# Kernel optimization log

Measured on AMD Instinct MI355X. Metric: run time of the kernel, lower is better.

Reference implementation:

```python
import jax, jax.numpy as jnp
import numpy as np

QUEST_DIM = 768
C, X, Y = 2048, 19, 19
B = 64

def setup_inputs() -> dict:
    key = jax.random.key(0)
    k1, k2, k3, k4 = jax.random.split(key, 4)
    text_fts = jax.random.normal(k1, (B, QUEST_DIM), dtype=jnp.float32)
    img_fts = jax.random.normal(k2, (B, C, X, Y), dtype=jnp.float32)
    # Linear params (PyTorch nn.Linear: y = x @ W.T + b)
    bound = 1.0 / np.sqrt(QUEST_DIM)
    W = jax.random.uniform(k3, (C, QUEST_DIM), minval=-bound, maxval=bound, dtype=jnp.float32)
    b = jax.random.uniform(k4, (C,), minval=-bound, maxval=bound, dtype=jnp.float32)
    return {"text_fts": text_fts, "img_fts": img_fts, "W": W, "b": b}

def reference(text_fts, img_fts, W, b):
    batch = text_fts.shape[0]
    q = text_fts @ W.T + b                      # [B, C]
    img_flat = img_fts.reshape(batch, C, X * Y) # [B, C, S]
    sims = jnp.einsum('bc,bcs->bs', q, img_flat)  # dot over channel dim
    weights = jax.nn.softmax(sims, axis=1)        # softmax over spatial locations
    final_ans = jnp.einsum('bcs,bs->bc', img_flat, weights)  # weighted pooling
    return final_ans
```

## Files before the change

### kernel.cpp

```cpp
#include <hip/hip_runtime.h>
#include <math.h>

#define Bsz  64
#define Cch  2048
#define Kdim 768
#define Ssp  361

__global__ __launch_bounds__(256) void k_qgemm(
    const float* __restrict__ text, const float* __restrict__ W,
    const float* __restrict__ bias, float* __restrict__ qT)
{
    const int lane = threadIdx.x & 63;
    const int wv   = threadIdx.x >> 6;
    const int c0   = blockIdx.x * 8 + wv * 2;
    const int b0   = blockIdx.y * 16;

    const float4* wA = (const float4*)(W + (size_t)c0 * Kdim);
    const float4* wB = (const float4*)(W + (size_t)(c0 + 1) * Kdim);
    const float4 a0 = wA[lane*3+0], a1 = wA[lane*3+1], a2 = wA[lane*3+2];
    const float4 b0v = wB[lane*3+0], b1v = wB[lane*3+1], b2v = wB[lane*3+2];
    const float biasA = bias[c0], biasB = bias[c0 + 1];

    for (int b = b0; b < b0 + 16; b++) {
        const float4* t = (const float4*)(text + (size_t)b * Kdim);
        const float4 t0 = t[lane*3+0], t1 = t[lane*3+1], t2 = t[lane*3+2];
        float r0 = a0.x*t0.x + a0.y*t0.y + a0.z*t0.z + a0.w*t0.w
                 + a1.x*t1.x + a1.y*t1.y + a1.z*t1.z + a1.w*t1.w
                 + a2.x*t2.x + a2.y*t2.y + a2.z*t2.z + a2.w*t2.w;
        float r1 = b0v.x*t0.x + b0v.y*t0.y + b0v.z*t0.z + b0v.w*t0.w
                 + b1v.x*t1.x + b1v.y*t1.y + b1v.z*t1.z + b1v.w*t1.w
                 + b2v.x*t2.x + b2v.y*t2.y + b2v.z*t2.z + b2v.w*t2.w;
        #pragma unroll
        for (int off = 32; off; off >>= 1) {
            r0 += __shfl_xor(r0, off);
            r1 += __shfl_xor(r1, off);
        }
        if (lane == 0) {
            qT[(size_t)c0 * Bsz + b]       = r0 + biasA;
            qT[(size_t)(c0 + 1) * Bsz + b] = r1 + biasB;
        }
    }
}

__global__ __launch_bounds__(384) void k_sims(
    const float* __restrict__ img, const float* __restrict__ qT,
    float* __restrict__ sims_part)
{
    const int b  = blockIdx.x;
    const int cg = blockIdx.y;
    const int tid = threadIdx.x;

    __shared__ float qL[128];
    if (tid < 128) qL[tid] = qT[(size_t)(cg * 128 + tid) * Bsz + b];
    __syncthreads();

    if (tid < Ssp) {
        const float* base = img + ((size_t)b * Cch + (size_t)cg * 128) * Ssp + tid;
        float acc = 0.f;
        #pragma unroll 8
        for (int c = 0; c < 128; c++)
            acc += qL[c] * base[(size_t)c * Ssp];
        sims_part[((size_t)b * 16 + cg) * Ssp + tid] = acc;
    }
}

__global__ __launch_bounds__(384) void k_wts(
    const float* __restrict__ sims_part, float* __restrict__ wts)
{
    const int b   = blockIdx.x;
    const int tid = threadIdx.x;
    const int lane = tid & 63;
    const int wv   = tid >> 6;

    __shared__ float red[6];

    float s0 = -1e30f;
    if (tid < Ssp) {
        float a = 0.f;
        #pragma unroll
        for (int g = 0; g < 16; g++)
            a += sims_part[((size_t)b * 16 + g) * Ssp + tid];
        s0 = a;
    }

    float m = s0;
    #pragma unroll
    for (int off = 32; off; off >>= 1) m = fmaxf(m, __shfl_xor(m, off));
    if (lane == 0) red[wv] = m;
    __syncthreads();
    m = red[0];
    #pragma unroll
    for (int w = 1; w < 6; w++) m = fmaxf(m, red[w]);
    __syncthreads();

    const float e0 = (tid < Ssp) ? __expf(s0 - m) : 0.f;
    float l = e0;
    #pragma unroll
    for (int off = 32; off; off >>= 1) l += __shfl_xor(l, off);
    if (lane == 0) red[wv] = l;
    __syncthreads();
    l = red[0] + red[1] + red[2] + red[3] + red[4] + red[5];

    if (tid < Ssp)
        wts[(size_t)b * Ssp + tid] = e0 / l;
}

__global__ __launch_bounds__(256) void k_pool(
    const float* __restrict__ img, const float* __restrict__ wts,
    float* __restrict__ out)
{
    const int b   = blockIdx.x;
    const int cg  = blockIdx.y;
    const int tid = threadIdx.x;
    const int lane = tid & 63;
    const int wv   = tid >> 6;

    __shared__ float w[Ssp];
    __shared__ float outL[64];

    if (tid < Ssp)       w[tid]       = wts[(size_t)b * Ssp + tid];
    if (tid + 256 < Ssp) w[tid + 256] = wts[(size_t)b * Ssp + tid + 256];
    __syncthreads();

    for (int c = wv; c < 64; c += 4) {
        const float* base = img + ((size_t)b * Cch + (size_t)cg * 64 + c) * Ssp;
        float p = 0.f;
        #pragma unroll
        for (int j = 0; j < 5; j++)
            p += base[lane + 64 * j] * w[lane + 64 * j];
        if (lane + 320 < Ssp)
            p += base[lane + 320] * w[lane + 320];
        #pragma unroll
        for (int off = 32; off; off >>= 1) p += __shfl_xor(p, off);
        if (lane == 0) outL[c] = p;
    }
    __syncthreads();
    if (tid < 64)
        out[(size_t)b * Cch + (size_t)cg * 64 + tid] = outL[tid];
}

extern "C" void kernel_launch(void* const* d_in, const int* in_sizes, int n_in,
                              void* d_out, int out_size, void* d_ws, size_t ws_size,
                              hipStream_t stream) {
    const float* text = (const float*)d_in[0];
    const float* img  = (const float*)d_in[1];
    const float* W    = (const float*)d_in[2];
    const float* bias = (const float*)d_in[3];
    float* out = (float*)d_out;

    float* qT        = (float*)d_ws;
    float* sims_part = qT + (size_t)Cch * Bsz;
    float* wts       = sims_part + (size_t)Bsz * 16 * Ssp;

    k_qgemm<<<dim3(256, 4), 256, 0, stream>>>(text, W, bias, qT);
    k_sims <<<dim3(Bsz, 16), 384, 0, stream>>>(img, qT, sims_part);
    k_wts  <<<dim3(Bsz),     384, 0, stream>>>(sims_part, wts);
    k_pool <<<dim3(Bsz, 32), 256, 0, stream>>>(img, wts, out);
}
```

Baseline: 318.7 us.

## Fuse softmax into sims kernel via last-block atomic counter; widen pool and qgemm grids

The softmax kernel is folded into the sims kernel: each block bumps a per-batch atomic counter, and the last of the 16 channel-group blocks reduces the partial sims and writes the softmax weights. This removes one kernel launch and its dependency gap, at the cost of a memset on the counters and threadfences. The qgemm grid is doubled so each block handles 8 batches instead of 16. The pool kernel moves to 512-thread blocks that each handle 128 channels, with two channels per wave iteration so each weight read from shared memory is reused.

```diff
diff --git a/kernel.cpp b/kernel.cpp
--- a/kernel.cpp
+++ b/kernel.cpp
@@ -13,7 +13,7 @@
     const int lane = threadIdx.x & 63;
     const int wv   = threadIdx.x >> 6;
     const int c0   = blockIdx.x * 8 + wv * 2;
-    const int b0   = blockIdx.y * 16;
+    const int b0   = blockIdx.y * 8;
 
     const float4* wA = (const float4*)(W + (size_t)c0 * Kdim);
     const float4* wB = (const float4*)(W + (size_t)(c0 + 1) * Kdim);
@@ -21,7 +21,7 @@
     const float4 b0v = wB[lane*3+0], b1v = wB[lane*3+1], b2v = wB[lane*3+2];
     const float biasA = bias[c0], biasB = bias[c0 + 1];
 
-    for (int b = b0; b < b0 + 16; b++) {
+    for (int b = b0; b < b0 + 8; b++) {
         const float4* t = (const float4*)(text + (size_t)b * Kdim);
         const float4 t0 = t[lane*3+0], t1 = t[lane*3+1], t2 = t[lane*3+2];
         float r0 = a0.x*t0.x + a0.y*t0.y + a0.z*t0.z + a0.w*t0.w
@@ -44,7 +44,8 @@
 
 __global__ __launch_bounds__(384) void k_sims(
     const float* __restrict__ img, const float* __restrict__ qT,
-    float* __restrict__ sims_part)
+    float* __restrict__ sims_part, float* __restrict__ wts,
+    int* __restrict__ cnt)
 {
     const int b  = blockIdx.x;
     const int cg = blockIdx.y;
@@ -62,16 +63,19 @@
             acc += qL[c] * base[(size_t)c * Ssp];
         sims_part[((size_t)b * 16 + cg) * Ssp + tid] = acc;
     }
-}
 
-__global__ __launch_bounds__(384) void k_wts(
-    const float* __restrict__ sims_part, float* __restrict__ wts)
-{
-    const int b   = blockIdx.x;
-    const int tid = threadIdx.x;
+    __syncthreads();
+    __shared__ int isLast;
+    if (tid == 0) {
+        __threadfence();
+        isLast = (atomicAdd(&cnt[b], 1) == 15);
+    }
+    __syncthreads();
+    if (!isLast) return;
+    __threadfence();
+
     const int lane = tid & 63;
     const int wv   = tid >> 6;
-
     __shared__ float red[6];
 
     float s0 = -1e30f;
@@ -105,7 +109,7 @@
         wts[(size_t)b * Ssp + tid] = e0 / l;
 }
 
-__global__ __launch_bounds__(256) void k_pool(
+__global__ __launch_bounds__(512) void k_pool(
     const float* __restrict__ img, const float* __restrict__ wts,
     float* __restrict__ out)
 {
@@ -116,27 +120,41 @@
     const int wv   = tid >> 6;
 
     __shared__ float w[Ssp];
-    __shared__ float outL[64];
+    __shared__ float outL[128];
 
-    if (tid < Ssp)       w[tid]       = wts[(size_t)b * Ssp + tid];
-    if (tid + 256 < Ssp) w[tid + 256] = wts[(size_t)b * Ssp + tid + 256];
+    if (tid < Ssp) w[tid] = wts[(size_t)b * Ssp + tid];
     __syncthreads();
 
-    for (int c = wv; c < 64; c += 4) {
-        const float* base = img + ((size_t)b * Cch + (size_t)cg * 64 + c) * Ssp;
-        float p = 0.f;
+    const int cbase = cg * 128 + wv * 16;
+    #pragma unroll 2
+    for (int cc = 0; cc < 16; cc += 2) {
+        const float* base0 = img + ((size_t)b * Cch + cbase + cc) * Ssp;
+        const float* base1 = base0 + Ssp;
+        float p0 = 0.f, p1 = 0.f;
         #pragma unroll
-        for (int j = 0; j < 5; j++)
-            p += base[lane + 64 * j] * w[lane + 64 * j];
-        if (lane + 320 < Ssp)
-            p += base[lane + 320] * w[lane + 320];
+        for (int j = 0; j < 5; j++) {
+            const float wj = w[lane + 64 * j];
+            p0 += base0[lane + 64 * j] * wj;
+            p1 += base1[lane + 64 * j] * wj;
+        }
+        if (lane + 320 < Ssp) {
+            const float wt = w[lane + 320];
+            p0 += base0[lane + 320] * wt;
+            p1 += base1[lane + 320] * wt;
+        }
         #pragma unroll
-        for (int off = 32; off; off >>= 1) p += __shfl_xor(p, off);
-        if (lane == 0) outL[c] = p;
+        for (int off = 32; off; off >>= 1) {
+            p0 += __shfl_xor(p0, off);
+            p1 += __shfl_xor(p1, off);
+        }
+        if (lane == 0) {
+            outL[wv * 16 + cc]     = p0;
+            outL[wv * 16 + cc + 1] = p1;
+        }
     }
     __syncthreads();
-    if (tid < 64)
-        out[(size_t)b * Cch + (size_t)cg * 64 + tid] = outL[tid];
+    if (tid < 128)
+        out[(size_t)b * Cch + cg * 128 + tid] = outL[tid];
 }
 
 extern "C" void kernel_launch(void* const* d_in, const int* in_sizes, int n_in,
@@ -151,9 +169,11 @@
     float* qT        = (float*)d_ws;
     float* sims_part = qT + (size_t)Cch * Bsz;
     float* wts       = sims_part + (size_t)Bsz * 16 * Ssp;
+    int*   cnt       = (int*)(wts + (size_t)Bsz * Ssp);
 
-    k_qgemm<<<dim3(256, 4), 256, 0, stream>>>(text, W, bias, qT);
-    k_sims <<<dim3(Bsz, 16), 384, 0, stream>>>(img, qT, sims_part);
-    k_wts  <<<dim3(Bsz),     384, 0, stream>>>(sims_part, wts);
-    k_pool <<<dim3(Bsz, 32), 256, 0, stream>>>(img, wts, out);
+    hipMemsetAsync(cnt, 0, Bsz * sizeof(int), stream);
+
+    k_qgemm<<<dim3(256, 8), 256, 0, stream>>>(text, W, bias, qT);
+    k_sims <<<dim3(Bsz, 16), 384, 0, stream>>>(img, qT, sims_part, wts, cnt);
+    k_pool <<<dim3(Bsz, 16), 512, 0, stream>>>(img, wts, out);
 }
```

Result: slower. 369.7 us (+16.0%).
